# Kernel tuning notes

Hardware: AMD Instinct MI355X
Metric: run time of the kernel (lower is better)

Reference implementation:

```python
import jax, jax.numpy as jnp
import numpy as np

XZ = jnp.array([0, 2])
XY = jnp.array([0, 1])
YZ = jnp.array([1, 2])


def _bilinear(plane, uv):
    """plane: (C,R,R) as (C,H,W); uv: (N,2) in [0,1], uv[:,0]->width, uv[:,1]->height.
    Border padding + align_corners=True semantics (grid_sample style)."""
    R = plane.shape[-1]
    xy = jnp.clip(uv, 0.0, 1.0) * (R - 1)
    x, y = xy[:, 0], xy[:, 1]
    x0 = jnp.floor(x)
    y0 = jnp.floor(y)
    x0i = jnp.clip(x0.astype(jnp.int32), 0, R - 1)
    y0i = jnp.clip(y0.astype(jnp.int32), 0, R - 1)
    x1i = jnp.clip(x0i + 1, 0, R - 1)
    y1i = jnp.clip(y0i + 1, 0, R - 1)
    wx = (x - x0)[None, :]  # (1,N)
    wy = (y - y0)[None, :]
    f00 = plane[:, y0i, x0i]  # (C,N)
    f01 = plane[:, y0i, x1i]
    f10 = plane[:, y1i, x0i]
    f11 = plane[:, y1i, x1i]
    top = f00 * (1.0 - wx) + f01 * wx
    bot = f10 * (1.0 - wx) + f11 * wx
    return (top * (1.0 - wy) + bot * wy).T  # (N,C)


def _sample_triplane(p, c_xz, c_xy, c_yz):
    """p: (bs,N,3) in [0,1]; planes: (bs,C,R,R). Returns (bs,N,C) summed over planes."""
    def per_batch(pb, fxz, fxy, fyz):
        return (_bilinear(fxz, pb[:, XZ])
                + _bilinear(fxy, pb[:, XY])
                + _bilinear(fyz, pb[:, YZ]))
    return jax.vmap(per_batch)(p, c_xz, c_xy, c_yz)


def setup_inputs() -> dict:
    key = jax.random.key(0)
    ks = jax.random.split(key, 12)
    bs, ns, C, S, R = 2, 50000, 32, 8, 128
    inp = {
        "query_pos": jax.random.uniform(ks[0], (bs, ns, 3), dtype=jnp.float32),
        "c_xz": jax.random.normal(ks[1], (bs, C, R, R), dtype=jnp.float32),
        "c_xy": jax.random.normal(ks[2], (bs, C, R, R), dtype=jnp.float32),
        "c_yz": jax.random.normal(ks[3], (bs, C, R, R), dtype=jnp.float32),
        # offset weights scaled small so sampled points stay mostly in-bounds
        "W_off": jax.random.normal(ks[4], (C, S * 3), dtype=jnp.float32) * 0.01,
        "b_off": jnp.zeros((S * 3,), dtype=jnp.float32),
        "W_w": jax.random.normal(ks[5], (C, S), dtype=jnp.float32) * 0.1,
        "b_w": jnp.zeros((S,), dtype=jnp.float32),
        "W_v": jax.random.normal(ks[6], (C, C), dtype=jnp.float32) * (1.0 / np.sqrt(C)),
        "b_v": jnp.zeros((C,), dtype=jnp.float32),
        "W_out": jax.random.normal(ks[7], (C, C), dtype=jnp.float32) * (1.0 / np.sqrt(C)),
        "b_out": jnp.zeros((C,), dtype=jnp.float32),
    }
    return inp


def reference(query_pos, c_xz, c_xy, c_yz, W_off, b_off, W_w, b_w, W_v, b_v, W_out, b_out):
    bs, ns, _ = query_pos.shape
    S = W_w.shape[1]
    # round 1: sample tri-plane features at query points
    feature = _sample_triplane(query_pos, c_xz, c_xy, c_yz)  # (bs,ns,C)
    # predict per-query sample offsets and weights
    off = (feature @ W_off + b_off).reshape(bs, ns, S, 3)
    w = (feature @ W_w + b_w).reshape(bs, ns, S, 1)
    pts = off + query_pos[:, :, None, :]  # (bs,ns,S,3)
    # round 2: sample at deformed points
    aux = _sample_triplane(pts.reshape(bs, ns * S, 3), c_xz, c_xy, c_yz)
    v = aux.reshape(bs, ns, S, -1) @ W_v + b_v  # (bs,ns,S,C)
    out = (v * w).sum(-2)                        # weighted reduce over samples
    out = out @ W_out + b_out + feature          # residual
    return out  # (bs,ns,C)
```

## Files before the change

kernel.cpp:

```cpp
#include <hip/hip_runtime.h>
#include <hip/hip_fp16.h>

#define BS 2
#define NS 50000
#define CCH 32
#define RR 128
#define SS 8

typedef float v2f __attribute__((ext_vector_type(2)));


__global__ __launch_bounds__(256)
void prep(const float* __restrict__ cxz,
          const float* __restrict__ cxy,
          const float* __restrict__ cyz,
          const float* __restrict__ Wv, const float* __restrict__ bv,
          const float* __restrict__ Wout,
          unsigned short* __restrict__ tp, float* __restrict__ Wc,
          float* __restrict__ bvw) {
    __shared__ float lds[32 * 129];
    int tid = threadIdx.x;
    int row = blockIdx.x;
    if (row < BS * 3 * RR) {
        int y  = row & 127;
        int pl = (row >> 7) % 3;
        int b  = row / 384;
        const float* src = (pl == 0) ? cxz : ((pl == 1) ? cxy : cyz);
        const float* sp = src + (((size_t)(b * CCH)) << 14) + (y << 7);
#pragma unroll
        for (int i = 0; i < 16; ++i) {
            int c = (tid >> 7) + 2 * i;
            int x = tid & 127;
            lds[c * 129 + x] = sp[((size_t)c << 14) + x];
        }
        __syncthreads();
        ushort2* dst = (ushort2*)(tp + ((size_t)row << 12));
#pragma unroll
        for (int i = 0; i < 8; ++i) {
            int c2 = tid & 15;
            int x  = (tid >> 4) + 16 * i;
            ushort2 v;
            v.x = __half_as_ushort(__float2half(lds[(2 * c2) * 129 + x]));
            v.y = __half_as_ushort(__float2half(lds[(2 * c2 + 1) * 129 + x]));
            dst[(x << 4) + c2] = v;
        }
    } else {
        int t = (row - BS * 3 * RR) * 256 + tid;
        int c = t >> 5, j = t & 31;
        float acc = 0.f;
#pragma unroll
        for (int k = 0; k < 32; ++k) acc += Wv[c * 32 + k] * Wout[k * 32 + j];
        Wc[t] = acc;
        if (t < 32) {
            float a2 = 0.f;
#pragma unroll
            for (int k = 0; k < 32; ++k) a2 += bv[k] * Wout[k * 32 + t];
            bvw[t] = a2;
        }
    }
}


struct f8 { v2f a[4]; };

struct Samp { uint4 u[12]; float f0, f1, f2; };

__device__ __forceinline__ void acc8(f8& acc, uint4 u, float w) {
    __half2 h0 = __builtin_bit_cast(__half2, u.x);
    __half2 h1 = __builtin_bit_cast(__half2, u.y);
    __half2 h2 = __builtin_bit_cast(__half2, u.z);
    __half2 h3 = __builtin_bit_cast(__half2, u.w);
    acc.a[0].x = fmaf(__half2float(h0.x), w, acc.a[0].x);
    acc.a[0].y = fmaf(__half2float(h0.y), w, acc.a[0].y);
    acc.a[1].x = fmaf(__half2float(h1.x), w, acc.a[1].x);
    acc.a[1].y = fmaf(__half2float(h1.y), w, acc.a[1].y);
    acc.a[2].x = fmaf(__half2float(h2.x), w, acc.a[2].x);
    acc.a[2].y = fmaf(__half2float(h2.y), w, acc.a[2].y);
    acc.a[3].x = fmaf(__half2float(h3.x), w, acc.a[3].x);
    acc.a[3].y = fmaf(__half2float(h3.y), w, acc.a[3].y);
}

__device__ __forceinline__ void axq(float p, int& i0, int& i1, float& w) {
    float x = fminf(fmaxf(p, 0.f), 1.f) * 127.f;
    float f = floorf(x);
    i0 = (int)f;
    i1 = min(i0 + 1, 127);
    w = x - f;
}

__device__ __forceinline__ Samp load_samp(const uint4* __restrict__ P0,
                                          float p0, float p1, float p2) {
    Samp t;
    int i00, i01, i10, i11, i20, i21;
    axq(p0, i00, i01, t.f0);
    axq(p1, i10, i11, t.f1);
    axq(p2, i20, i21, t.f2);
    const uint4* Pxz = P0;
    const uint4* Pxy = P0 + (1 << 16);
    const uint4* Pyz = P0 + (2 << 16);
    int c00 = i00 << 2, c01 = i01 << 2;
    int c10 = i10 << 2, c11 = i11 << 2;
    int r10 = i10 << 9, r11 = i11 << 9;
    int r20 = i20 << 9, r21 = i21 << 9;
    t.u[0]  = Pxz[r20 + c00];  t.u[1]  = Pxz[r20 + c01];
    t.u[2]  = Pxz[r21 + c00];  t.u[3]  = Pxz[r21 + c01];
    t.u[4]  = Pxy[r10 + c00];  t.u[5]  = Pxy[r10 + c01];
    t.u[6]  = Pxy[r11 + c00];  t.u[7]  = Pxy[r11 + c01];
    t.u[8]  = Pyz[r20 + c10];  t.u[9]  = Pyz[r20 + c11];
    t.u[10] = Pyz[r21 + c10];  t.u[11] = Pyz[r21 + c11];
    return t;
}

__device__ __forceinline__ void eval_plane(f8& acc, const uint4* u,
                                           float wx, float wy) {
    float w11 = wx * wy;
    float w01 = wx - w11;
    float w10 = wy - w11;
    float w00 = 1.f - wx - w10;
    acc8(acc, u[0], w00);
    acc8(acc, u[1], w01);
    acc8(acc, u[2], w10);
    acc8(acc, u[3], w11);
}

__device__ __forceinline__ void eval_samp(const Samp& t, f8& acc) {
    eval_plane(acc, t.u + 0, t.f0, t.f2);
    eval_plane(acc, t.u + 4, t.f0, t.f1);
    eval_plane(acc, t.u + 8, t.f1, t.f2);
}

#define GETE(v, idx) (((idx) & 1) ? (v).a[((idx) >> 1) & 3].y : (v).a[((idx) >> 1) & 3].x)
#define GETC(v, idx) __shfl(GETE(v, idx), base | ((idx) >> 3), 64)

__global__ __launch_bounds__(128)
void eda_main(const float* __restrict__ qp, const unsigned short* __restrict__ tp,
              const float* __restrict__ Woff, const float* __restrict__ boff,
              const float* __restrict__ Ww, const float* __restrict__ bw,
              const float* __restrict__ Wc, const float* __restrict__ bvw,
              const float* __restrict__ bout, float* __restrict__ out) {
    __shared__ v2f sWcat[32][4][4];
    __shared__ v2f sWc[32][4][4];
    __shared__ float sbcat[32];
    __shared__ float sbvw[32];
    __shared__ float sbout[32];

    int tid = threadIdx.x;
    int lane = tid & 3;
    int base = tid & 60;
    int b  = blockIdx.x & 1;
    int qi = (blockIdx.x >> 1) * 32 + (tid >> 2);
    int qq = min(qi, NS - 1);

    const float* p = qp + ((size_t)b * NS + qq) * 3;
    float p0 = p[0], p1 = p[1], p2 = p[2];

    const uint4* P0 = (const uint4*)tp + (((size_t)(b * 3)) << 16) + lane;

    Samp fs = load_samp(P0, p0, p1, p2);

    for (int i = tid; i < 1024; i += 128) {
        int k = i >> 5, j = i & 31;
        ((float*)sWcat)[i] = (j < 24) ? Woff[k * 24 + j] : Ww[k * 8 + (j - 24)];
        ((float*)sWc)[i]   = Wc[i];
    }
    if (tid < 32) {
        sbcat[tid] = (tid < 24) ? boff[tid] : bw[tid - 24];
        sbvw[tid]  = bvw[tid];
        sbout[tid] = bout[tid];
    }
    __syncthreads();

    f8 feat = {};
    eval_samp(fs, feat);

    f8 cat;
#pragma unroll
    for (int e = 0; e < 4; ++e) {
        cat.a[e].x = sbcat[(lane << 3) + 2 * e];
        cat.a[e].y = sbcat[(lane << 3) + 2 * e + 1];
    }
#pragma unroll
    for (int k = 0; k < 32; ++k) {
        float fc = GETC(feat, k);
        v2f fc2 = {fc, fc};
#pragma unroll
        for (int e = 0; e < 4; ++e)
            cat.a[e] = __builtin_elementwise_fma(fc2, sWcat[k][lane][e], cat.a[e]);
    }

    f8 wa = {};
    float wsum = 0.f;
    float w_cur = GETC(cat, 24);
    Samp cur = load_samp(P0, p0 + GETC(cat, 0), p1 + GETC(cat, 1), p2 + GETC(cat, 2));
    Samp nxt;
    float w_nxt;
#pragma unroll
    for (int s = 0; s < SS; ++s) {
        if (s < SS - 1) {
            w_nxt = GETC(cat, 24 + (s + 1));
            nxt = load_samp(P0, p0 + GETC(cat, 3 * (s + 1) + 0),
                                p1 + GETC(cat, 3 * (s + 1) + 1),
                                p2 + GETC(cat, 3 * (s + 1) + 2));
        }
        f8 aux = {};
        eval_samp(cur, aux);
        v2f w2 = {w_cur, w_cur};
#pragma unroll
        for (int e = 0; e < 4; ++e)
            wa.a[e] = __builtin_elementwise_fma(w2, aux.a[e], wa.a[e]);
        wsum += w_cur;
        if (s < SS - 1) { cur = nxt; w_cur = w_nxt; }
    }

    f8 o;
    v2f ws2 = {wsum, wsum};
#pragma unroll
    for (int e = 0; e < 4; ++e) {
        v2f bo  = {sbout[(lane << 3) + 2 * e], sbout[(lane << 3) + 2 * e + 1]};
        v2f bv2 = {sbvw[(lane << 3) + 2 * e], sbvw[(lane << 3) + 2 * e + 1]};
        o.a[e] = __builtin_elementwise_fma(ws2, bv2, bo) + feat.a[e];
    }
#pragma unroll
    for (int k = 0; k < 32; ++k) {
        float wc = GETC(wa, k);
        v2f wc2 = {wc, wc};
#pragma unroll
        for (int e = 0; e < 4; ++e)
            o.a[e] = __builtin_elementwise_fma(wc2, sWc[k][lane][e], o.a[e]);
    }

    if (qi < NS) {
        float* dst = out + ((size_t)b * NS + qi) * 32 + (lane << 3);
        *(float4*)dst       = make_float4(o.a[0].x, o.a[0].y, o.a[1].x, o.a[1].y);
        *(float4*)(dst + 4) = make_float4(o.a[2].x, o.a[2].y, o.a[3].x, o.a[3].y);
    }
}

extern "C" void kernel_launch(void* const* d_in, const int* in_sizes, int n_in,
                              void* d_out, int out_size, void* d_ws, size_t ws_size,
                              hipStream_t stream) {
    const float* qp   = (const float*)d_in[0];
    const float* cxz  = (const float*)d_in[1];
    const float* cxy  = (const float*)d_in[2];
    const float* cyz  = (const float*)d_in[3];
    const float* Woff = (const float*)d_in[4];
    const float* boff = (const float*)d_in[5];
    const float* Ww   = (const float*)d_in[6];
    const float* bw   = (const float*)d_in[7];
    const float* Wv   = (const float*)d_in[8];
    const float* bv   = (const float*)d_in[9];
    const float* Wout = (const float*)d_in[10];
    const float* bout = (const float*)d_in[11];
    float* out = (float*)d_out;

    unsigned short* tp = (unsigned short*)d_ws;
    float* Wc  = (float*)((char*)d_ws + (size_t)BS * 3 * RR * RR * CCH * 2);
    float* bvw = Wc + 1024;

    prep<<<BS * 3 * RR + 4, 256, 0, stream>>>(cxz, cxy, cyz, Wv, bv, Wout, tp, Wc, bvw);
    int blocks_per_batch = (NS + 31) / 32;
    eda_main<<<2 * blocks_per_batch, 128, 0, stream>>>(qp, tp, Woff, boff, Ww, bw,
                                                       Wc, bvw, bout, out);
}
```

Measured before the change: 139.1 us.

## Split each query across 8 lanes, halving per-lane bilinear corner loads

Each query now runs on 8 lanes instead of 4. The two lane halves each fetch two of the four bilinear corners per plane and combine their partial sums with an xor-shuffle, so the prefetched sample state per lane drops from 12 to 6 uint4 values. The final matmuls are also split, so each lane computes 4 output channels, and the block grows to 256 threads. The aim is to cut register pressure and raise occupancy and memory-level parallelism. In exchange it adds shuffles and duplicates the index arithmetic across lanes. Clamping the low index to 126 gives the same result at the border, since the weight becomes 1 on the upper corner.

```diff
diff --git a/kernel.cpp b/kernel.cpp
--- a/kernel.cpp
+++ b/kernel.cpp
@@ -62,8 +62,8 @@
 
 
 struct f8 { v2f a[4]; };
-
-struct Samp { uint4 u[12]; float f0, f1, f2; };
+struct c4 { v2f a[2]; };
+struct Samp { uint4 u[6]; float f0, f1, f2; };
 
 __device__ __forceinline__ void acc8(f8& acc, uint4 u, float w) {
     __half2 h0 = __builtin_bit_cast(__half2, u.x);
@@ -80,88 +80,96 @@
     acc.a[3].y = fmaf(__half2float(h3.y), w, acc.a[3].y);
 }
 
-__device__ __forceinline__ void axq(float p, int& i0, int& i1, float& w) {
+__device__ __forceinline__ void axq(float p, int& i0, float& w) {
     float x = fminf(fmaxf(p, 0.f), 1.f) * 127.f;
-    float f = floorf(x);
-    i0 = (int)f;
-    i1 = min(i0 + 1, 127);
-    w = x - f;
-}
-
-__device__ __forceinline__ Samp load_samp(const uint4* __restrict__ P0,
-                                          float p0, float p1, float p2) {
+    i0 = min((int)x, 126);
+    w = x - (float)i0;
+}
+
+__device__ __forceinline__ Samp load_samp(const uint4* __restrict__ Pxz,
+                                          float p0, float p1, float p2, int hi) {
     Samp t;
-    int i00, i01, i10, i11, i20, i21;
-    axq(p0, i00, i01, t.f0);
-    axq(p1, i10, i11, t.f1);
-    axq(p2, i20, i21, t.f2);
-    const uint4* Pxz = P0;
-    const uint4* Pxy = P0 + (1 << 16);
-    const uint4* Pyz = P0 + (2 << 16);
-    int c00 = i00 << 2, c01 = i01 << 2;
-    int c10 = i10 << 2, c11 = i11 << 2;
-    int r10 = i10 << 9, r11 = i11 << 9;
-    int r20 = i20 << 9, r21 = i21 << 9;
-    t.u[0]  = Pxz[r20 + c00];  t.u[1]  = Pxz[r20 + c01];
-    t.u[2]  = Pxz[r21 + c00];  t.u[3]  = Pxz[r21 + c01];
-    t.u[4]  = Pxy[r10 + c00];  t.u[5]  = Pxy[r10 + c01];
-    t.u[6]  = Pxy[r11 + c00];  t.u[7]  = Pxy[r11 + c01];
-    t.u[8]  = Pyz[r20 + c10];  t.u[9]  = Pyz[r20 + c11];
-    t.u[10] = Pyz[r21 + c10];  t.u[11] = Pyz[r21 + c11];
+    int i00, i10, i20;
+    axq(p0, i00, t.f0);
+    axq(p1, i10, t.f1);
+    axq(p2, i20, t.f2);
+    int i01 = i00 + 1, i11 = i10 + 1, i21 = i20 + 1;
+    int cF0 = hi ? i01 : i00,  cS0 = hi ? i00 : i01;
+    int cF1 = hi ? i11 : i10,  cS1 = hi ? i10 : i11;
+    const uint4* Pxy = Pxz + (1 << 16);
+    const uint4* Pyz = Pxz + (2 << 16);
+    t.u[0] = Pxz[(i20 << 9) + (cF0 << 2)];
+    t.u[1] = Pxz[(i21 << 9) + (cS0 << 2)];
+    t.u[2] = Pxy[(i10 << 9) + (cF0 << 2)];
+    t.u[3] = Pxy[(i11 << 9) + (cS0 << 2)];
+    t.u[4] = Pyz[(i20 << 9) + (cF1 << 2)];
+    t.u[5] = Pyz[(i21 << 9) + (cS1 << 2)];
     return t;
 }
 
-__device__ __forceinline__ void eval_plane(f8& acc, const uint4* u,
-                                           float wx, float wy) {
+__device__ __forceinline__ void eval_plane(f8& acc, uint4 ua, uint4 ub,
+                                           float wx, float wy, int hi) {
     float w11 = wx * wy;
     float w01 = wx - w11;
     float w10 = wy - w11;
     float w00 = 1.f - wx - w10;
-    acc8(acc, u[0], w00);
-    acc8(acc, u[1], w01);
-    acc8(acc, u[2], w10);
-    acc8(acc, u[3], w11);
-}
-
-__device__ __forceinline__ void eval_samp(const Samp& t, f8& acc) {
-    eval_plane(acc, t.u + 0, t.f0, t.f2);
-    eval_plane(acc, t.u + 4, t.f0, t.f1);
-    eval_plane(acc, t.u + 8, t.f1, t.f2);
-}
-
-#define GETE(v, idx) (((idx) & 1) ? (v).a[((idx) >> 1) & 3].y : (v).a[((idx) >> 1) & 3].x)
-#define GETC(v, idx) __shfl(GETE(v, idx), base | ((idx) >> 3), 64)
-
-__global__ __launch_bounds__(128)
+    float wF = hi ? w01 : w00;
+    float wS = hi ? w10 : w11;
+    acc8(acc, ua, wF);
+    acc8(acc, ub, wS);
+}
+
+__device__ __forceinline__ void eval_samp(const Samp& t, f8& acc, int hi) {
+    eval_plane(acc, t.u[0], t.u[1], t.f0, t.f2, hi);
+    eval_plane(acc, t.u[2], t.u[3], t.f0, t.f1, hi);
+    eval_plane(acc, t.u[4], t.u[5], t.f1, t.f2, hi);
+}
+
+__device__ __forceinline__ void reduce8(f8& v) {
+#pragma unroll
+    for (int e = 0; e < 4; ++e) {
+        v.a[e].x += __shfl_xor(v.a[e].x, 4, 64);
+        v.a[e].y += __shfl_xor(v.a[e].y, 4, 64);
+    }
+}
+
+#define GETE8(v, idx) (((idx) & 1) ? (v).a[((idx) >> 1) & 3].y : (v).a[((idx) >> 1) & 3].x)
+#define GETC8(v, idx) __shfl(GETE8(v, idx), base | ((idx) >> 3), 64)
+#define GETE4(v, idx) (((idx) & 1) ? (v).a[((idx) >> 1) & 1].y : (v).a[((idx) >> 1) & 1].x)
+#define GETC4(v, idx) __shfl(GETE4(v, idx), base | (((idx) & 4)) | ((idx) >> 3), 64)
+
+__global__ __launch_bounds__(256)
 void eda_main(const float* __restrict__ qp, const unsigned short* __restrict__ tp,
               const float* __restrict__ Woff, const float* __restrict__ boff,
               const float* __restrict__ Ww, const float* __restrict__ bw,
               const float* __restrict__ Wc, const float* __restrict__ bvw,
               const float* __restrict__ bout, float* __restrict__ out) {
-    __shared__ v2f sWcat[32][4][4];
-    __shared__ v2f sWc[32][4][4];
+    __shared__ float sWcat[32][32];
+    __shared__ float sWc2[32][32];
     __shared__ float sbcat[32];
     __shared__ float sbvw[32];
     __shared__ float sbout[32];
 
     int tid = threadIdx.x;
-    int lane = tid & 3;
-    int base = tid & 60;
+    int lane = tid & 7;
+    int base = tid & 56;
+    int hi   = (lane >> 2) & 1;
+    int jofs = ((lane & 3) << 3) + (hi << 2);
     int b  = blockIdx.x & 1;
-    int qi = (blockIdx.x >> 1) * 32 + (tid >> 2);
+    int qi = (blockIdx.x >> 1) * 32 + (tid >> 3);
     int qq = min(qi, NS - 1);
 
     const float* p = qp + ((size_t)b * NS + qq) * 3;
     float p0 = p[0], p1 = p[1], p2 = p[2];
 
-    const uint4* P0 = (const uint4*)tp + (((size_t)(b * 3)) << 16) + lane;
-
-    Samp fs = load_samp(P0, p0, p1, p2);
-
-    for (int i = tid; i < 1024; i += 128) {
+    const uint4* P0 = (const uint4*)tp + (((size_t)(b * 3)) << 16) + (lane & 3);
+
+    Samp fs = load_samp(P0, p0, p1, p2, hi);
+
+    for (int i = tid; i < 1024; i += 256) {
         int k = i >> 5, j = i & 31;
         ((float*)sWcat)[i] = (j < 24) ? Woff[k * 24 + j] : Ww[k * 8 + (j - 24)];
-        ((float*)sWc)[i]   = Wc[i];
+        ((float*)sWc2)[i]  = Wc[i];
     }
     if (tid < 32) {
         sbcat[tid] = (tid < 24) ? boff[tid] : bw[tid - 24];
@@ -171,39 +179,39 @@
     __syncthreads();
 
     f8 feat = {};
-    eval_samp(fs, feat);
-
-    f8 cat;
-#pragma unroll
-    for (int e = 0; e < 4; ++e) {
-        cat.a[e].x = sbcat[(lane << 3) + 2 * e];
-        cat.a[e].y = sbcat[(lane << 3) + 2 * e + 1];
-    }
+    eval_samp(fs, feat, hi);
+    reduce8(feat);
+
+    c4 cat;
+    cat.a[0] = *(const v2f*)&sbcat[jofs];
+    cat.a[1] = *(const v2f*)&sbcat[jofs + 2];
 #pragma unroll
     for (int k = 0; k < 32; ++k) {
-        float fc = GETC(feat, k);
+        float fc = GETC8(feat, k);
+        const v2f* wp = (const v2f*)&sWcat[k][jofs];
         v2f fc2 = {fc, fc};
-#pragma unroll
-        for (int e = 0; e < 4; ++e)
-            cat.a[e] = __builtin_elementwise_fma(fc2, sWcat[k][lane][e], cat.a[e]);
+        cat.a[0] = __builtin_elementwise_fma(fc2, wp[0], cat.a[0]);
+        cat.a[1] = __builtin_elementwise_fma(fc2, wp[1], cat.a[1]);
     }
 
     f8 wa = {};
     float wsum = 0.f;
-    float w_cur = GETC(cat, 24);
-    Samp cur = load_samp(P0, p0 + GETC(cat, 0), p1 + GETC(cat, 1), p2 + GETC(cat, 2));
+    float w_cur = GETC4(cat, 24);
+    Samp cur = load_samp(P0, p0 + GETC4(cat, 0), p1 + GETC4(cat, 1),
+                         p2 + GETC4(cat, 2), hi);
     Samp nxt;
     float w_nxt;
 #pragma unroll
     for (int s = 0; s < SS; ++s) {
         if (s < SS - 1) {
-            w_nxt = GETC(cat, 24 + (s + 1));
-            nxt = load_samp(P0, p0 + GETC(cat, 3 * (s + 1) + 0),
-                                p1 + GETC(cat, 3 * (s + 1) + 1),
-                                p2 + GETC(cat, 3 * (s + 1) + 2));
+            w_nxt = GETC4(cat, 24 + (s + 1));
+            nxt = load_samp(P0, p0 + GETC4(cat, 3 * (s + 1) + 0),
+                                p1 + GETC4(cat, 3 * (s + 1) + 1),
+                                p2 + GETC4(cat, 3 * (s + 1) + 2), hi);
         }
         f8 aux = {};
-        eval_samp(cur, aux);
+        eval_samp(cur, aux, hi);
+        reduce8(aux);
         v2f w2 = {w_cur, w_cur};
 #pragma unroll
         for (int e = 0; e < 4; ++e)
@@ -212,27 +220,30 @@
         if (s < SS - 1) { cur = nxt; w_cur = w_nxt; }
     }
 
-    f8 o;
+    c4 o;
     v2f ws2 = {wsum, wsum};
-#pragma unroll
-    for (int e = 0; e < 4; ++e) {
-        v2f bo  = {sbout[(lane << 3) + 2 * e], sbout[(lane << 3) + 2 * e + 1]};
-        v2f bv2 = {sbvw[(lane << 3) + 2 * e], sbvw[(lane << 3) + 2 * e + 1]};
-        o.a[e] = __builtin_elementwise_fma(ws2, bv2, bo) + feat.a[e];
+    {
+        v2f bo0 = *(const v2f*)&sbout[jofs];
+        v2f bo1 = *(const v2f*)&sbout[jofs + 2];
+        v2f bv0 = *(const v2f*)&sbvw[jofs];
+        v2f bv1 = *(const v2f*)&sbvw[jofs + 2];
+        v2f fA = hi ? feat.a[2] : feat.a[0];
+        v2f fB = hi ? feat.a[3] : feat.a[1];
+        o.a[0] = __builtin_elementwise_fma(ws2, bv0, bo0) + fA;
+        o.a[1] = __builtin_elementwise_fma(ws2, bv1, bo1) + fB;
     }
 #pragma unroll
     for (int k = 0; k < 32; ++k) {
-        float wc = GETC(wa, k);
+        float wc = GETC8(wa, k);
+        const v2f* wp = (const v2f*)&sWc2[k][jofs];
         v2f wc2 = {wc, wc};
-#pragma unroll
-        for (int e = 0; e < 4; ++e)
-            o.a[e] = __builtin_elementwise_fma(wc2, sWc[k][lane][e], o.a[e]);
+        o.a[0] = __builtin_elementwise_fma(wc2, wp[0], o.a[0]);
+        o.a[1] = __builtin_elementwise_fma(wc2, wp[1], o.a[1]);
     }
 
     if (qi < NS) {
-        float* dst = out + ((size_t)b * NS + qi) * 32 + (lane << 3);
-        *(float4*)dst       = make_float4(o.a[0].x, o.a[0].y, o.a[1].x, o.a[1].y);
-        *(float4*)(dst + 4) = make_float4(o.a[2].x, o.a[2].y, o.a[3].x, o.a[3].y);
+        float* dst = out + ((size_t)b * NS + qi) * 32 + jofs;
+        *(float4*)dst = make_float4(o.a[0].x, o.a[0].y, o.a[1].x, o.a[1].y);
     }
 }
 
@@ -259,6 +270,6 @@
 
     prep<<<BS * 3 * RR + 4, 256, 0, stream>>>(cxz, cxy, cyz, Wv, bv, Wout, tp, Wc, bvw);
     int blocks_per_batch = (NS + 31) / 32;
-    eda_main<<<2 * blocks_per_batch, 128, 0, stream>>>(qp, tp, Woff, boff, Ww, bw,
+    eda_main<<<2 * blocks_per_batch, 256, 0, stream>>>(qp, tp, Woff, boff, Ww, bw,
                                                        Wc, bvw, bout, out);
 }
```

New measurement: 138.2 us. No clear change (-0.6%).
